# Performance work log

Measured on AMD Instinct MI355X. Metric: run time of the kernel, lower is better.

Reference implementation:

```python
import jax, jax.numpy as jnp
import numpy as np


def setup_inputs() -> dict:
    key = jax.random.key(0)
    k1, k2, k3, k4 = jax.random.split(key, 4)
    B, C_in, C_out, H, W = 8, 256, 256, 160, 160
    mask = jax.random.randint(k1, (B, 1, H, W), 0, 2, dtype=jnp.int32)  # binary hard mask
    ori = jax.random.normal(k2, (B, C_in, H, W), dtype=jnp.float32)
    weight = jax.random.normal(k3, (C_out, C_in, 3, 3), dtype=jnp.float32) * 0.02
    bias = jax.random.normal(k4, (C_out,), dtype=jnp.float32) * 0.02
    return {"mask": mask, "ori": ori, "weight": weight, "bias": bias}


def reference(mask, ori, weight, bias):
    # apply_mask: broadcast binary [B,1,H,W] mask over channels, zero masked regions
    x = ori * mask.astype(ori.dtype)
    # dense 3x3 conv, stride 1, padding 1 (SAME) -> output [B, C_out, H, W]
    out = jax.lax.conv_general_dilated(
        x, weight,
        window_strides=(1, 1),
        padding='SAME',
        dimension_numbers=('NCHW', 'OIHW', 'NCHW'),
    )
    return out + bias[None, :, None, None]
```

## Files before the change

### kernel.cpp

```cpp
#include <hip/hip_runtime.h>

typedef __attribute__((ext_vector_type(8))) short short8;
typedef __attribute__((ext_vector_type(4))) float f32x4;

#define B_    8
#define CI    256
#define CO    256
#define Hh    160
#define Ww    160
#define HP    162
#define WP    162
#define HWp   (Hh * Ww)
#define XPAD_ELEMS (B_ * HP * WP * CI)
#define W3_ELEMS   (9 * CI * CO)
#define NT    36
#define BSLOT (160 * 64)

#define NBORD 644
#define NPW   2304
#define NPX   (B_ * Hh * 4 * 3)

__device__ __forceinline__ unsigned short f2bf(float f) {
  unsigned int u = __float_as_uint(f);
  u += 0x7FFFu + ((u >> 16) & 1u);
  return (unsigned short)(u >> 16);
}

__global__ void prep_all(const float* __restrict__ ori, const int* __restrict__ mask,
                         const float* __restrict__ w,
                         unsigned short* __restrict__ xp, unsigned short* __restrict__ w3) {
  __shared__ float tile[64][65];
  const int bid = blockIdx.x;
  const int t = threadIdx.x;

  if (bid < NBORD) {
    int g = bid * 256 + t;
    int pos = g >> 5;
    int c = (g & 31) << 3;
    int n = pos / 644;
    int p = pos - n * 644;
    int y, x;
    if (p < 324) { y = (p < 162) ? 0 : 161; x = (p < 162) ? p : p - 162; }
    else { int q = p - 324; y = 1 + (q >> 1); x = (q & 1) ? 161 : 0; }
    unsigned short* d = xp + (((size_t)(n * 162 + y)) * 162 + x) * 256 + c;
    *(uint4*)d = (uint4){0u, 0u, 0u, 0u};
    return;
  }
  if (bid < NBORD + NPW) {
    int i = (bid - NBORD) * 256 + t;
    int e = i & 7, l = (i >> 3) & 63, g = i >> 9;
    int mi = g & 1, wm = (g >> 1) & 3, kk = (g >> 3) & 1;
    int qm = (g >> 4) & 1, cic = (g >> 5) & 3, shift = g >> 7;
    int co = qm * 128 + wm * 32 + mi * 16 + (l & 15);
    int ci = cic * 64 + kk * 32 + (l >> 4) * 8 + e;
    w3[i] = f2bf(w[(co * 256 + ci) * 9 + shift]);
    return;
  }

  int bid2 = bid - (NBORD + NPW);
  int wt = bid2 % 3;
  int t1 = bid2 / 3;
  int cit = t1 & 3;
  int t2 = t1 >> 2;
  int h = t2 % Hh;
  int n = t2 / Hh;

  int wl = t & 63;
  int ww = wt * 64 + wl;
  bool valid = (ww < Ww);
  float m = 0.f;
  if (valid) m = (float)mask[(n * Hh + h) * Ww + ww];
  const float* src = ori + (((size_t)(n * CI + cit * 64) * Hh + h) * Ww + ww);
  int r0 = t >> 6;
#pragma unroll
  for (int k = 0; k < 16; ++k) {
    int ci_l = r0 * 16 + k;
    float v = 0.f;
    if (valid) v = src[(size_t)ci_l * HWp] * m;
    tile[ci_l][wl] = v;
  }
  __syncthreads();

  int wl2 = t >> 2;
  int wo = wt * 64 + wl2;
  if (wo < Ww) {
    int cseg = (t & 3) * 16;
    union { unsigned short u[8]; uint4 v; } p0, p1;
#pragma unroll
    for (int j = 0; j < 8; ++j) p0.u[j] = f2bf(tile[cseg + j][wl2]);
#pragma unroll
    for (int j = 0; j < 8; ++j) p1.u[j] = f2bf(tile[cseg + 8 + j][wl2]);
    unsigned short* dst = xp + ((size_t)((n * HP + h + 1) * WP) + (wo + 1)) * CI + cit * 64 + cseg;
    *(uint4*)dst = p0.v;
    *(uint4*)(dst + 8) = p1.v;
  }
}

__device__ __forceinline__ void gload16(const unsigned short* g, unsigned short* l) {
  __builtin_amdgcn_global_load_lds((const __attribute__((address_space(1))) void*)g,
                                   (__attribute__((address_space(3))) void*)l, 16, 0, 0);
}

__global__ void __launch_bounds__(256, 2)
sconv_gemm(const unsigned short* __restrict__ xp, const unsigned short* __restrict__ w3,
           const float* __restrict__ bias, float* __restrict__ out) {
  __shared__ unsigned short Bs[3][BSLOT];

  const int bid = blockIdx.x;
  const int n = bid & 7;
  const int rest = bid >> 3;
  const int cohalf = rest & 1;
  const int h = rest >> 1;

  const int t = threadIdx.x;
  const int l = t & 63;
  const int wv = t >> 6;
  const int wm = wv >> 1;
  const int wn = wv & 1;

  const int lr = l >> 3;
  const int swz8 = ((l & 7) ^ lr) << 3;
  const int lc = l & 15, hi4 = l >> 4, lx7 = l & 7;
  const unsigned xrow = (unsigned)(n * HP + h);

  unsigned boff[5];
#pragma unroll
  for (int k = 0; k < 5; ++k)
    boff[k] = (unsigned)(k * 32 + wv * 8 + lr) * 256 + swz8;

  f32x4 acc[4][5];
#pragma unroll
  for (int j = 0; j < 4; ++j)
#pragma unroll
    for (int ni = 0; ni < 5; ++ni)
      acc[j][ni] = (f32x4){0.f, 0.f, 0.f, 0.f};

  short8 aK0[4], aK1[4], bb[5];

#define TPAR(ts, cic, sh, kh, kw)                                             \
  const int cic = ((ts) * 57) >> 9;                                           \
  const int sh = (ts) - cic * 9;                                              \
  const int kh = (sh * 11) >> 5;                                              \
  const int kw = sh - kh * 3;

  auto STG = [&](int ts, unsigned short* slot, int k) {
    TPAR(ts, cic, sh, kh, kw)
    (void)sh;
    const unsigned short* src = xp + ((size_t)(xrow + kh) * WP + kw) * 256 + (cic << 6) + boff[k];
    gload16(src, slot + (k * 32 + wv * 8) * 64);
  };

  auto AGH = [&](int ts, int kk, short8* dst) {
    TPAR(ts, cic, sh, kh, kw)
    (void)kh; (void)kw;
    const unsigned short* p = w3 +
        ((size_t)(sh * 128 + cic * 32 + cohalf * 16 + kk * 8 + wm * 4) << 9) + (l << 3);
#pragma unroll
    for (int j = 0; j < 4; ++j)
      dst[j] = *(const short8*)(p + (j << 9));
  };

#define BBR(slot, kk) do {                                                    \
  _Pragma("unroll")                                                           \
  for (int i = 0; i < 5; ++i)                                                 \
    bb[i] = *(const short8*)((slot) + ((wn * 80 + i * 16 + lc) * 64) +        \
                             (((((kk) << 2) + hi4) ^ lx7) << 3));             \
} while (0)

#define CL(AH) do {                                                           \
  __builtin_amdgcn_s_setprio(1);                                              \
  _Pragma("unroll")                                                           \
  for (int j = 0; j < 4; ++j)                                                 \
    _Pragma("unroll")                                                         \
    for (int i = 0; i < 5; ++i)                                               \
      acc[j][i] = __builtin_amdgcn_mfma_f32_16x16x32_bf16(                    \
          AH[j], bb[i], acc[j][i], 0, 0, 0);                                  \
  __builtin_amdgcn_s_setprio(0);                                              \
} while (0)

#define PH(slot, kk, AH, ISSUES, ENDW) do {                                   \
  ISSUES                                                                      \
  BBR(slot, kk);                                                              \
  __builtin_amdgcn_s_barrier();                                               \
  CL(AH);                                                                     \
  ENDW                                                                        \
  __builtin_amdgcn_s_barrier();                                               \
} while (0)

#define TILE(tt, sc, sn) do {                                                 \
  PH(sc, 0, aK0,                                                              \
     { STG((tt) + 2, sn, 0); STG((tt) + 2, sn, 1); STG((tt) + 2, sn, 2); },   \
     {});                                                                     \
  PH(sc, 1, aK1,                                                              \
     { AGH((tt) + 1, 0, aK0); STG((tt) + 2, sn, 3); STG((tt) + 2, sn, 4); },  \
     { AGH((tt) + 1, 1, aK1);                                                 \
       asm volatile("s_waitcnt vmcnt(13)" ::: "memory"); });                  \
} while (0)

  unsigned short* const s0 = &Bs[0][0];
  unsigned short* const s1 = &Bs[1][0];
  unsigned short* const s2 = &Bs[2][0];

  for (int k = 0; k < 5; ++k) STG(0, s0, k);
  for (int k = 0; k < 5; ++k) STG(1, s1, k);
  AGH(0, 0, aK0);
  AGH(0, 1, aK1);
  asm volatile("s_waitcnt vmcnt(13)" ::: "memory");
  __builtin_amdgcn_s_barrier();

  for (int t3 = 0; t3 < 33; t3 += 3) {
    TILE(t3 + 0, s0, s2);
    TILE(t3 + 1, s1, s0);
    TILE(t3 + 2, s2, s1);
  }
  TILE(33, s0, s2);
  PH(s1, 0, aK0, {}, {});
  PH(s1, 1, aK1, { AGH(35, 0, aK0); },
     { AGH(35, 1, aK1);
       asm volatile("s_waitcnt vmcnt(8)" ::: "memory"); });
  PH(s2, 0, aK0, {}, {});
  {
    BBR(s2, 1);
    CL(aK1);
  }

#pragma unroll
  for (int j = 0; j < 4; ++j) {
    int cobase = cohalf * 128 + wm * 64 + j * 16 + hi4 * 4;
    const float4 bv = *(const float4*)(bias + cobase);
    float* op = out + (((size_t)n * CO + cobase) * Hh + h) * Ww;
#pragma unroll
    for (int ni = 0; ni < 5; ++ni) {
      int w = wn * 80 + ni * 16 + lc;
      f32x4 v = acc[j][ni];
      op[w]                   = v[0] + bv.x;
      op[(size_t)HWp + w]     = v[1] + bv.y;
      op[(size_t)2 * HWp + w] = v[2] + bv.z;
      op[(size_t)3 * HWp + w] = v[3] + bv.w;
    }
  }
}

extern "C" void kernel_launch(void* const* d_in, const int* in_sizes, int n_in,
                              void* d_out, int out_size, void* d_ws, size_t ws_size,
                              hipStream_t stream) {
  const int* mask = (const int*)d_in[0];
  const float* ori = (const float*)d_in[1];
  const float* weight = (const float*)d_in[2];
  const float* bias = (const float*)d_in[3];
  float* out = (float*)d_out;

  unsigned short* xp = (unsigned short*)d_ws;
  unsigned short* w3 = xp + XPAD_ELEMS;

  prep_all<<<NBORD + NPW + NPX, 256, 0, stream>>>(ori, mask, weight, xp, w3);
  sconv_gemm<<<2560, 256, 0, stream>>>(xp, w3, bias, out);
}
```

Before: 339.3 us.

## Merge both output-channel halves into one 512-thread block sharing the input tile

Each block now covers all 256 output channels for one output row using 8 waves instead of 4, so the staged input tile in LDS is loaded once and shared by both channel halves. The grid is halved and the staging loads are spread over 8 waves, with uneven wait counts per wave group. This cuts global and LDS staging traffic for the input, but doubles the threads per block and may lower occupancy or raise register pressure under launch bounds of 512 threads with 2 blocks.

```diff
diff --git a/kernel.cpp b/kernel.cpp
--- a/kernel.cpp
+++ b/kernel.cpp
@@ -101,21 +101,19 @@
                                    (__attribute__((address_space(3))) void*)l, 16, 0, 0);
 }
 
-__global__ void __launch_bounds__(256, 2)
+__global__ void __launch_bounds__(512, 2)
 sconv_gemm(const unsigned short* __restrict__ xp, const unsigned short* __restrict__ w3,
            const float* __restrict__ bias, float* __restrict__ out) {
   __shared__ unsigned short Bs[3][BSLOT];
 
   const int bid = blockIdx.x;
   const int n = bid & 7;
-  const int rest = bid >> 3;
-  const int cohalf = rest & 1;
-  const int h = rest >> 1;
+  const int h = bid >> 3;
 
   const int t = threadIdx.x;
   const int l = t & 63;
   const int wv = t >> 6;
-  const int wm = wv >> 1;
+  const int q = wv >> 1;
   const int wn = wv & 1;
 
   const int lr = l >> 3;
@@ -123,10 +121,7 @@
   const int lc = l & 15, hi4 = l >> 4, lx7 = l & 7;
   const unsigned xrow = (unsigned)(n * HP + h);
 
-  unsigned boff[5];
-#pragma unroll
-  for (int k = 0; k < 5; ++k)
-    boff[k] = (unsigned)(k * 32 + wv * 8 + lr) * 256 + swz8;
+  const unsigned boff0 = (unsigned)(wv * 8 + lr) * 256 + swz8;
 
   f32x4 acc[4][5];
 #pragma unroll
@@ -143,18 +138,21 @@
   const int kh = (sh * 11) >> 5;                                              \
   const int kw = sh - kh * 3;
 
-  auto STG = [&](int ts, unsigned short* slot, int k) {
+  auto STG = [&](int ts, unsigned short* slot) {
     TPAR(ts, cic, sh, kh, kw)
     (void)sh;
-    const unsigned short* src = xp + ((size_t)(xrow + kh) * WP + kw) * 256 + (cic << 6) + boff[k];
-    gload16(src, slot + (k * 32 + wv * 8) * 64);
+    const unsigned short* src = xp + ((size_t)(xrow + kh) * WP + kw) * 256 + (cic << 6) + boff0;
+    unsigned short* dst = slot + (wv * 8) * 64;
+    gload16(src, dst);
+    gload16(src + 64 * 256, dst + 64 * 64);
+    if (wv < 4) gload16(src + 128 * 256, dst + 128 * 64);
   };
 
   auto AGH = [&](int ts, int kk, short8* dst) {
     TPAR(ts, cic, sh, kh, kw)
     (void)kh; (void)kw;
     const unsigned short* p = w3 +
-        ((size_t)(sh * 128 + cic * 32 + cohalf * 16 + kk * 8 + wm * 4) << 9) + (l << 3);
+        ((size_t)(sh * 128 + cic * 32 + (q >> 1) * 16 + kk * 8 + (q & 1) * 4) << 9) + (l << 3);
 #pragma unroll
     for (int j = 0; j < 4; ++j)
       dst[j] = *(const short8*)(p + (j << 9));
@@ -187,25 +185,26 @@
   __builtin_amdgcn_s_barrier();                                               \
 } while (0)
 
+#define TILEWAIT do {                                                         \
+  if (wv < 4) asm volatile("s_waitcnt vmcnt(11)" ::: "memory");               \
+  else        asm volatile("s_waitcnt vmcnt(10)" ::: "memory");               \
+} while (0)
+
 #define TILE(tt, sc, sn) do {                                                 \
-  PH(sc, 0, aK0,                                                              \
-     { STG((tt) + 2, sn, 0); STG((tt) + 2, sn, 1); STG((tt) + 2, sn, 2); },   \
-     {});                                                                     \
-  PH(sc, 1, aK1,                                                              \
-     { AGH((tt) + 1, 0, aK0); STG((tt) + 2, sn, 3); STG((tt) + 2, sn, 4); },  \
-     { AGH((tt) + 1, 1, aK1);                                                 \
-       asm volatile("s_waitcnt vmcnt(13)" ::: "memory"); });                  \
+  PH(sc, 0, aK0, { STG((tt) + 2, sn); }, {});                                 \
+  PH(sc, 1, aK1, { AGH((tt) + 1, 0, aK0); },                                  \
+     { AGH((tt) + 1, 1, aK1); TILEWAIT; });                                   \
 } while (0)
 
   unsigned short* const s0 = &Bs[0][0];
   unsigned short* const s1 = &Bs[1][0];
   unsigned short* const s2 = &Bs[2][0];
 
-  for (int k = 0; k < 5; ++k) STG(0, s0, k);
-  for (int k = 0; k < 5; ++k) STG(1, s1, k);
+  STG(0, s0);
+  STG(1, s1);
   AGH(0, 0, aK0);
   AGH(0, 1, aK1);
-  asm volatile("s_waitcnt vmcnt(13)" ::: "memory");
+  asm volatile("s_waitcnt vmcnt(0)" ::: "memory");
   __builtin_amdgcn_s_barrier();
 
   for (int t3 = 0; t3 < 33; t3 += 3) {
@@ -226,7 +225,7 @@
 
 #pragma unroll
   for (int j = 0; j < 4; ++j) {
-    int cobase = cohalf * 128 + wm * 64 + j * 16 + hi4 * 4;
+    int cobase = q * 64 + j * 16 + hi4 * 4;
     const float4 bv = *(const float4*)(bias + cobase);
     float* op = out + (((size_t)n * CO + cobase) * Hh + h) * Ww;
 #pragma unroll
@@ -254,5 +253,5 @@
   unsigned short* w3 = xp + XPAD_ELEMS;
 
   prep_all<<<NBORD + NPW + NPX, 256, 0, stream>>>(ori, mask, weight, xp, w3);
-  sconv_gemm<<<2560, 256, 0, stream>>>(xp, w3, bias, out);
-}
+  sconv_gemm<<<1280, 512, 0, stream>>>(xp, w3, bias, out);
+}
```

Result: slower. 368.3 us (+8.6%).
